# Optimization experiments

Measured on AMD Instinct MI355X. Metric: run time of the kernel, lower is better.

Reference implementation:

```python
import jax, jax.numpy as jnp
import numpy as np

N_NODES = 100000
N_EDGES = 1600000
IN_DIM = 128
HID = 128
OUT_DIM = 64
EPS = 1e-8


def setup_inputs() -> dict:
    key = jax.random.key(0)
    ks = jax.random.split(key, 10)
    x = jax.random.normal(ks[0], (N_NODES, IN_DIM), dtype=jnp.float32)
    edge_index = jax.random.randint(ks[1], (2, N_EDGES), 0, N_NODES, dtype=jnp.int64)
    edge_attr = jax.random.uniform(ks[2], (N_EDGES, 4), dtype=jnp.float32)
    s1 = 1.0 / np.sqrt(IN_DIM)
    s2 = 1.0 / np.sqrt(HID)
    sr = 1.0 / np.sqrt(2 * HID)
    W1 = jax.random.normal(ks[3], (HID, IN_DIM), dtype=jnp.float32) * s1
    b1 = jnp.zeros((HID,), dtype=jnp.float32)
    W2 = jax.random.normal(ks[4], (HID, HID), dtype=jnp.float32) * s2
    b2 = jnp.zeros((HID,), dtype=jnp.float32)
    Wr = jax.random.normal(ks[5], (OUT_DIM, 2 * HID), dtype=jnp.float32) * sr
    br = jnp.zeros((OUT_DIM,), dtype=jnp.float32)
    return {"x": x, "edge_index": edge_index, "edge_attr": edge_attr,
            "W1": W1, "b1": b1, "W2": W2, "b2": b2, "Wr": Wr, "br": br}


def _edge_weight_from_attr_auto(edge_attr):
    # mean over features, min-max normalize, invert, clamp >= 0
    m = edge_attr.mean(axis=-1)                      # [E]
    m_min, m_max = m.min(), m.max()
    m_norm = (m - m_min) / (m_max - m_min + EPS)
    w = jnp.where(m_max - m_min > EPS, 1.0 - m_norm, jnp.ones_like(m))
    return jnp.clip(w, 0.0)


def reference(x, edge_index, edge_attr, W1, b1, W2, b2, Wr, br):
    N = x.shape[0]
    row, col = edge_index[0], edge_index[1]          # source -> target
    ew = _edge_weight_from_attr_auto(edge_attr)      # [E]
    # GCN normalization with self-loops (self-loop weight = 1.0)
    deg = jax.ops.segment_sum(ew, col, num_segments=N) + 1.0   # [N]
    dis = jax.lax.rsqrt(deg)                         # deg >= 1
    norm = dis[row] * ew * dis[col]                  # [E]

    def gcn(h, W, b):
        hW = h @ W.T                                 # [N, d_out]
        agg = jax.ops.segment_sum(norm[:, None] * hW[row], col, num_segments=N)
        # self-loop contribution: dis[i] * 1.0 * dis[i] * hW[i]
        return agg + (dis * dis)[:, None] * hW + b

    # dropout in eval mode -> identity
    h1 = jax.nn.relu(gcn(x, W1, b1))                 # [N, HID]
    h2 = jax.nn.relu(gcn(h1, W2, b2))                # [N, HID]
    hcat = jnp.concatenate([h1, h2], axis=-1)        # [N, 2*HID] (JK concat)
    return hcat @ Wr.T + br                          # residue-level [N, OUT_DIM]
```

## Files before the change

### kernel.cpp

```cpp
#include <hip/hip_runtime.h>

#define NN 100000
#define NE 1600000
#define HID 128
#define ODIM 64
#define NBK 196
#define BSHIFT 9
#define BGRID 512
#define CVTB 48
#define CHUNK 3125
#define BITER 13
#define BINCAP 12288
#define SMAX 4504
#define LMAX 568

typedef unsigned int u32;
typedef unsigned short u16;
typedef __bf16 bf16x8 __attribute__((ext_vector_type(8)));
typedef float f32x4 __attribute__((ext_vector_type(4)));
typedef float f32x2 __attribute__((ext_vector_type(2)));

__device__ __forceinline__ float bf_lo(u32 p){ return __uint_as_float(p << 16); }
__device__ __forceinline__ float bf_hi(u32 p){ return __uint_as_float(p & 0xffff0000u); }
__device__ __forceinline__ u16 f2bf(float f){
  u32 u = __float_as_uint(f);
  u += 0x7fffu + ((u >> 16) & 1u);
  return (u16)(u >> 16);
}
__device__ __forceinline__ bf16x8 ld8bf(const u16* p){ return *(const bf16x8*)p; }
__device__ __forceinline__ bf16x8 cvt8(const float* p){
  union { bf16x8 v; u16 s[8]; } r;
#pragma unroll
  for (int i = 0; i < 8; i++) r.s[i] = f2bf(p[i]);
  return r.v;
}

__global__ __launch_bounds__(256) void k_bin(
    const float* __restrict__ eattr, const int* __restrict__ erow,
    const int* __restrict__ ecol, u32* __restrict__ bcur,
    uint2* __restrict__ bin, u32* __restrict__ minmax,
    const float* __restrict__ W1, const float* __restrict__ W2,
    const float* __restrict__ Wr, u16* __restrict__ W1b,
    u16* __restrict__ W2b, u16* __restrict__ Wrb){
  int tid = threadIdx.x;
  if (blockIdx.x >= BGRID){
    int i = (blockIdx.x - BGRID) * 256 + tid;
    const float* src; u16* dst; int off;
    if (i < 4096){ src = W1; dst = W1b; off = i; }
    else if (i < 8192){ src = W2; dst = W2b; off = i - 4096; }
    else { src = Wr; dst = Wrb; off = i - 8192; }
    float4 v = ((const float4*)src)[off];
    uint2 o;
    o.x = (u32)f2bf(v.x) | ((u32)f2bf(v.y) << 16);
    o.y = (u32)f2bf(v.z) | ((u32)f2bf(v.w) << 16);
    ((uint2*)dst)[off] = o;
    return;
  }
  __shared__ u32 lcnt[NBK], lofs[NBK], gb[NBK];
  __shared__ u32 scn[256];
  __shared__ u16 lmap[LMAX];
  __shared__ uint2 stage[SMAX];
  __shared__ u32 Tt;
  __shared__ float smin[4], smax[4];
  for (int t = tid; t < NBK; t += 256) lcnt[t] = 0;
  __syncthreads();
  int base = blockIdx.x * CHUNK;
  float lmin = __uint_as_float(0x7f800000u), lmax = 0.f;
  u32 pk[BITER]; float mv[BITER]; u32 sv[BITER];
#pragma unroll
  for (int it = 0; it < BITER; it++){
    int idx = it * 256 + tid;
    u32 p = 0xFFFFFFFFu; float m = 0.f; u32 s = 0;
    if (idx < CHUNK){
      int e = base + idx;
      float4 a = ((const float4*)eattr)[e];
      m = 0.25f * (a.x + a.y + a.z + a.w);
      lmin = fminf(lmin, m); lmax = fmaxf(lmax, m);
      int c = ecol[e];
      s = (u32)erow[e]; if (s >= NN) s = 0;
      if ((u32)c < NN){
        u32 b = (u32)c >> BSHIFT;
        u32 r = atomicAdd(&lcnt[b], 1u);
        p = (b << 21) | (((u32)c & 511u) << 12) | r;
      }
    }
    pk[it] = p; mv[it] = m; sv[it] = s;
  }
  __syncthreads();
  u32 na = 0, n = 0;
  if (tid < NBK){ n = lcnt[tid]; na = (n + 7u) & ~7u; }
  scn[tid] = na; __syncthreads();
  for (int s = 1; s < 256; s <<= 1){
    u32 t = (tid >= s) ? scn[tid - s] : 0;
    __syncthreads();
    scn[tid] += t;
    __syncthreads();
  }
  u32 ex = scn[tid] - na;
  if (tid < NBK){
    lofs[tid] = ex;
    u32 g = 0x80000000u;
    if (na){
      u32 gl = atomicAdd(&bcur[tid], na);
      if (gl + na <= BINCAP) g = (u32)tid * BINCAP + gl;
    }
    gb[tid] = g;
    for (u32 l = ex >> 3; l < (ex + na) >> 3; l++) lmap[l] = (u16)tid;
    uint2 sent; sent.x = 0xFFFFFFFFu; sent.y = 0u;
    for (u32 k = n; k < na; k++) stage[ex + k] = sent;
  }
  if (tid == 255) Tt = scn[255];
  __syncthreads();
#pragma unroll
  for (int it = 0; it < BITER; it++){
    u32 p = pk[it];
    if (p == 0xFFFFFFFFu) continue;
    uint2 rec; rec.x = sv[it] | (((p >> 12) & 511u) << 17); rec.y = __float_as_uint(mv[it]);
    stage[lofs[p >> 21] + (p & 4095u)] = rec;
  }
  __syncthreads();
  u32 T = Tt;
  for (u32 i = tid; i < T; i += 256){
    u32 b = lmap[i >> 3];
    u32 g = gb[b];
    if (g != 0x80000000u) bin[g + (i - lofs[b])] = stage[i];
  }
  for (int off = 32; off; off >>= 1){
    lmin = fminf(lmin, __shfl_xor(lmin, off));
    lmax = fmaxf(lmax, __shfl_xor(lmax, off));
  }
  int wid = tid >> 6, lane = tid & 63;
  if (lane == 0){ smin[wid] = lmin; smax[wid] = lmax; }
  __syncthreads();
  if (tid == 0){
    float mn = fminf(fminf(smin[0], smin[1]), fminf(smin[2], smin[3]));
    float mx = fmaxf(fmaxf(smax[0], smax[1]), fmaxf(smax[2], smax[3]));
    atomicMax(&minmax[0], ~__float_as_uint(mn));
    atomicMax(&minmax[1], __float_as_uint(mx));
  }
}

__global__ __launch_bounds__(1024) void k_sort(
    const u32* __restrict__ bcur, const uint2* __restrict__ bin,
    const u32* __restrict__ minmax, u32* __restrict__ csr,
    int* __restrict__ row_start, int* __restrict__ counts, float* __restrict__ dis){
  int b = blockIdx.x;
  int bb = b * BINCAP, be = bb + (int)bcur[b];
  float mn  = __uint_as_float(~minmax[0]);
  float mx  = __uint_as_float(minmax[1]);
  float rng = mx - mn;
  bool flat = !(rng > 1e-8f);
  float inv = 1.f / (rng + 1e-8f);
  __shared__ u32 cnt[512], off[512], cur[512], degfx[512];
  int tid = threadIdx.x;
  if (tid < 512){ cnt[tid] = 0; degfx[tid] = 0; }
  __syncthreads();
  for (int i = bb + tid; i < be; i += 1024){
    uint2 r = bin[i];
    if (r.x == 0xFFFFFFFFu) continue;
    u32 d = (r.x >> 17) & 511u;
    float w = flat ? 1.f : fmaxf(1.f - (__uint_as_float(r.y) - mn) * inv, 0.f);
    atomicAdd(&cnt[d], 1u);
    atomicAdd(&degfx[d], (u32)(w * 1048576.f + 0.5f));
  }
  __syncthreads();
  u32 v = 0;
  if (tid < 512){ v = cnt[tid]; off[tid] = v; }
  __syncthreads();
  for (int s = 1; s < 512; s <<= 1){
    u32 t = 0;
    if (tid < 512 && tid >= s) t = off[tid - s];
    __syncthreads();
    if (tid < 512) off[tid] += t;
    __syncthreads();
  }
  if (tid < 512){
    u32 ex = off[tid] - v;
    cur[tid] = ex;
    int node = (b << BSHIFT) + tid;
    if (node < NN){
      row_start[node] = bb + (int)ex;
      counts[node] = (int)v;
      dis[node] = rsqrtf(1.f + (float)degfx[tid] * (1.f / 1048576.f));
    }
  }
  __syncthreads();
  for (int i = bb + tid; i < be; i += 1024){
    uint2 r = bin[i];
    if (r.x == 0xFFFFFFFFu) continue;
    u32 d = (r.x >> 17) & 511u;
    float w = flat ? 1.f : fmaxf(1.f - (__uint_as_float(r.y) - mn) * inv, 0.f);
    u32 wq = (u32)(w * 32767.f + 0.5f);
    u32 pos = (u32)bb + atomicAdd(&cur[d], 1u);
    csr[pos] = (r.x & 0x1FFFFu) | (wq << 17);
  }
}

template <bool A_F32>
__global__ __launch_bounds__(256) void k_gemm128(
    const void* __restrict__ Av, const u16* __restrict__ Bt,
    const float* __restrict__ dis, u16* __restrict__ G){
  int wave = threadIdx.x >> 6, lane = threadIdx.x & 63;
  int m0 = blockIdx.x * 32;
  int m = lane & 15, q = lane >> 4;
  const float* a0f = (const float*)Av + (size_t)(m0 + m) * HID;
  const float* a1f = a0f + (size_t)16 * HID;
  const u16*   a0b = (const u16*)Av   + (size_t)(m0 + m) * HID;
  const u16*   a1b = a0b + (size_t)16 * HID;
  const u16* brow0 = Bt + (size_t)(wave * 16 + m) * HID;
  const u16* brow1 = brow0 + (size_t)64 * HID;
  f32x4 acc00 = {0.f,0.f,0.f,0.f}, acc01 = {0.f,0.f,0.f,0.f};
  f32x4 acc10 = {0.f,0.f,0.f,0.f}, acc11 = {0.f,0.f,0.f,0.f};
#pragma unroll
  for (int kb = 0; kb < HID; kb += 32){
    bf16x8 af0 = A_F32 ? cvt8(a0f + kb + q * 8) : ld8bf(a0b + kb + q * 8);
    bf16x8 af1 = A_F32 ? cvt8(a1f + kb + q * 8) : ld8bf(a1b + kb + q * 8);
    bf16x8 bf0 = ld8bf(brow0 + kb + q * 8);
    bf16x8 bf1 = ld8bf(brow1 + kb + q * 8);
    acc00 = __builtin_amdgcn_mfma_f32_16x16x32_bf16(af0, bf0, acc00, 0, 0, 0);
    acc01 = __builtin_amdgcn_mfma_f32_16x16x32_bf16(af0, bf1, acc01, 0, 0, 0);
    acc10 = __builtin_amdgcn_mfma_f32_16x16x32_bf16(af1, bf0, acc10, 0, 0, 0);
    acc11 = __builtin_amdgcn_mfma_f32_16x16x32_bf16(af1, bf1, acc11, 0, 0, 0);
  }
  u16* crow0 = G + (size_t)(m0 + q * 4) * HID + wave * 16 + m;
  u16* crow1 = crow0 + (size_t)16 * HID;
#pragma unroll
  for (int r = 0; r < 4; r++){
    float d0 = dis[m0 + q * 4 + r];
    float d1 = dis[m0 + 16 + q * 4 + r];
    crow0[(size_t)r * HID]      = f2bf(acc00[r] * d0);
    crow0[(size_t)r * HID + 64] = f2bf(acc01[r] * d0);
    crow1[(size_t)r * HID]      = f2bf(acc10[r] * d1);
    crow1[(size_t)r * HID + 64] = f2bf(acc11[r] * d1);
  }
}

__global__ __launch_bounds__(256) void k_aggregate(
    const int* __restrict__ row_start, const int* __restrict__ counts,
    const u32* __restrict__ csr, const float* __restrict__ dis,
    const u16* __restrict__ g, const float* __restrict__ bias,
    u16* __restrict__ hout){
  int node = blockIdx.x * 4 + (threadIdx.x >> 6);
  int lane = threadIdx.x & 63;
  int s = row_start[node], c = counts[node];
  const u32* gp = (const u32*)g;
  u32 sv = gp[((size_t)node << 6) + lane];
  f32x2 acc = {bf_lo(sv), bf_hi(sv)};
  for (int base = 0; base < c; base += 64){
    int nch = min(64, c - base);
    u32 sidx = 0; float ws = 0.f;
    if (lane < nch){
      u32 pw = csr[s + base + lane];
      sidx = pw & 0x1FFFFu;
      ws = (float)(pw >> 17) * (1.f / 32767.f);
    }
    u32 wsb = __float_as_uint(ws);
    int j = 0;
#define GATH(T) \
    for (; j + T <= nch; j += T){ \
      u32 pv[T]; float wv[T]; \
      _Pragma("unroll") \
      for (int t = 0; t < T; t++){ \
        u32 st = (u32)__builtin_amdgcn_readlane(sidx, j + t); \
        wv[t] = __uint_as_float(__builtin_amdgcn_readlane(wsb, j + t)); \
        const u32* rowp = gp + st * 64u;          \
        pv[t] = rowp[lane]; \
      } \
      _Pragma("unroll") \
      for (int t = 0; t < T; t++){ \
        f32x2 val = {bf_lo(pv[t]), bf_hi(pv[t])}; \
        acc += wv[t] * val; \
      } \
    }
    GATH(16)
    GATH(8)
    GATH(4)
#undef GATH
    for (; j < nch; ++j){
      u32 st = (u32)__builtin_amdgcn_readlane(sidx, j);
      float wt = __uint_as_float(__builtin_amdgcn_readlane(wsb, j));
      const u32* rowp = gp + st * 64u;
      u32 pv = rowp[lane];
      f32x2 val = {bf_lo(pv), bf_hi(pv)};
      acc += wt * val;
    }
  }
  float di = dis[node];
  float2 bv = ((const float2*)bias)[lane];
  float o0 = fmaxf(acc.x * di + bv.x, 0.f);
  float o1 = fmaxf(acc.y * di + bv.y, 0.f);
  ((u32*)hout)[((size_t)node << 6) + lane] = (u32)f2bf(o0) | ((u32)f2bf(o1) << 16);
}

__global__ __launch_bounds__(256) void k_readout(
    const u16* __restrict__ h1, const u16* __restrict__ h2,
    const u16* __restrict__ Wrb, const float* __restrict__ br, float* __restrict__ out){
  int wave = threadIdx.x >> 6, lane = threadIdx.x & 63;
  int m0 = blockIdx.x * 32;
  int n0 = wave * 16;
  int m = lane & 15, q = lane >> 4;
  const u16* a10 = h1 + (size_t)(m0 + m) * HID;
  const u16* a11 = a10 + (size_t)16 * HID;
  const u16* a20 = h2 + (size_t)(m0 + m) * HID;
  const u16* a21 = a20 + (size_t)16 * HID;
  const u16* b  = Wrb + (size_t)(n0 + m) * (2 * HID);
  f32x4 acc0 = {0.f,0.f,0.f,0.f}, acc1 = {0.f,0.f,0.f,0.f};
#pragma unroll
  for (int kb = 0; kb < HID; kb += 32){
    bf16x8 bf = ld8bf(b + kb + q * 8);
    acc0 = __builtin_amdgcn_mfma_f32_16x16x32_bf16(ld8bf(a10 + kb + q * 8), bf, acc0, 0, 0, 0);
    acc1 = __builtin_amdgcn_mfma_f32_16x16x32_bf16(ld8bf(a11 + kb + q * 8), bf, acc1, 0, 0, 0);
  }
#pragma unroll
  for (int kb = 0; kb < HID; kb += 32){
    bf16x8 bf = ld8bf(b + HID + kb + q * 8);
    acc0 = __builtin_amdgcn_mfma_f32_16x16x32_bf16(ld8bf(a20 + kb + q * 8), bf, acc0, 0, 0, 0);
    acc1 = __builtin_amdgcn_mfma_f32_16x16x32_bf16(ld8bf(a21 + kb + q * 8), bf, acc1, 0, 0, 0);
  }
  float bias = br[n0 + m];
  float* crow0 = out + (size_t)(m0 + q * 4) * ODIM + n0 + m;
  float* crow1 = crow0 + (size_t)16 * ODIM;
#pragma unroll
  for (int r = 0; r < 4; r++){
    crow0[(size_t)r * ODIM] = acc0[r] + bias;
    crow1[(size_t)r * ODIM] = acc1[r] + bias;
  }
}

extern "C" void kernel_launch(void* const* d_in, const int* in_sizes, int n_in,
                              void* d_out, int out_size, void* d_ws, size_t ws_size,
                              hipStream_t stream){
  const float* x     = (const float*)d_in[0];
  const int*   eidx  = (const int*)d_in[1];
  const float* eattr = (const float*)d_in[2];
  const float* W1    = (const float*)d_in[3];
  const float* b1    = (const float*)d_in[4];
  const float* W2    = (const float*)d_in[5];
  const float* b2    = (const float*)d_in[6];
  const float* Wr    = (const float*)d_in[7];
  const float* br    = (const float*)d_in[8];
  const int* erow  = eidx;
  const int* ecol  = eidx + NE;

  char* w = (char*)d_ws;
  auto carve = [&](size_t bytes) -> void* {
    void* p = (void*)w;
    w += (bytes + 255) & ~(size_t)255;
    return p;
  };
  u32* csr       = (u32*)carve((size_t)NBK * BINCAP * 4);
  u32* bcur      = (u32*)carve(256 * 4);
  u32* minmax    = (u32*)carve(256);
  int* row_start = (int*)carve((size_t)NN * 4);
  int* counts    = (int*)carve((size_t)NN * 4);
  float* dis     = (float*)carve((size_t)NN * 4);
  u16* W1b       = (u16*)carve((size_t)HID * HID * 2);
  u16* W2b       = (u16*)carve((size_t)HID * HID * 2);
  u16* Wrb       = (u16*)carve((size_t)ODIM * 2 * HID * 2);
  u16* g         = (u16*)carve((size_t)NN * HID * 2);
  u16* h1        = (u16*)carve((size_t)NN * HID * 2);
  u16* h2        = (u16*)carve((size_t)NN * HID * 2);
  uint2* bin     = (uint2*)h2;

  hipMemsetAsync(bcur, 0, 1024 + 256, stream);
  k_bin<<<BGRID + CVTB, 256, 0, stream>>>(eattr, erow, ecol, bcur, bin, minmax,
                                          W1, W2, Wr, W1b, W2b, Wrb);
  k_sort<<<NBK, 1024, 0, stream>>>(bcur, bin, minmax, csr, row_start, counts, dis);

  k_gemm128<true><<<NN / 32, 256, 0, stream>>>(x, W1b, dis, g);
  k_aggregate<<<NN / 4, 256, 0, stream>>>(row_start, counts, csr, dis, g, b1, h1);
  k_gemm128<false><<<NN / 32, 256, 0, stream>>>(h1, W2b, dis, g);
  k_aggregate<<<NN / 4, 256, 0, stream>>>(row_start, counts, csr, dis, g, b2, h2);
  k_readout<<<NN / 32, 256, 0, stream>>>(h1, h2, Wrb, br, (float*)d_out);
}
```

Measured before the change: 386.3 us.

## Slice feature matrices into 16-column planes for cache-local gathers in aggregation

The intermediate g, h1 and h2 buffers are stored as 8 column slices of 16 bf16 values each ([8][N][16]), and the GEMM and readout kernels read and write this sliced layout. Each aggregation block handles one slice for 16 nodes, and each wave splits 8 edges across lane groups of 8 lanes before combining partial sums with cross-lane shuffles. The aim is to shrink the working set of each gather pass so the randomly gathered rows stay in L2/MALL. In exchange, the CSR list is read 8 times and extra shuffle reductions are added.

```diff
diff --git a/kernel.cpp b/kernel.cpp
--- a/kernel.cpp
+++ b/kernel.cpp
@@ -18,7 +18,6 @@
 typedef unsigned short u16;
 typedef __bf16 bf16x8 __attribute__((ext_vector_type(8)));
 typedef float f32x4 __attribute__((ext_vector_type(4)));
-typedef float f32x2 __attribute__((ext_vector_type(2)));
 
 __device__ __forceinline__ float bf_lo(u32 p){ return __uint_as_float(p << 16); }
 __device__ __forceinline__ float bf_hi(u32 p){ return __uint_as_float(p & 0xffff0000u); }
@@ -34,6 +33,7 @@
   for (int i = 0; i < 8; i++) r.s[i] = f2bf(p[i]);
   return r.v;
 }
+
 
 __global__ __launch_bounds__(256) void k_bin(
     const float* __restrict__ eattr, const int* __restrict__ erow,
@@ -205,33 +205,38 @@
   int m = lane & 15, q = lane >> 4;
   const float* a0f = (const float*)Av + (size_t)(m0 + m) * HID;
   const float* a1f = a0f + (size_t)16 * HID;
-  const u16*   a0b = (const u16*)Av   + (size_t)(m0 + m) * HID;
-  const u16*   a1b = a0b + (size_t)16 * HID;
+  const u16* Ab = (const u16*)Av;
   const u16* brow0 = Bt + (size_t)(wave * 16 + m) * HID;
   const u16* brow1 = brow0 + (size_t)64 * HID;
   f32x4 acc00 = {0.f,0.f,0.f,0.f}, acc01 = {0.f,0.f,0.f,0.f};
   f32x4 acc10 = {0.f,0.f,0.f,0.f}, acc11 = {0.f,0.f,0.f,0.f};
 #pragma unroll
   for (int kb = 0; kb < HID; kb += 32){
-    bf16x8 af0 = A_F32 ? cvt8(a0f + kb + q * 8) : ld8bf(a0b + kb + q * 8);
-    bf16x8 af1 = A_F32 ? cvt8(a1f + kb + q * 8) : ld8bf(a1b + kb + q * 8);
-    bf16x8 bf0 = ld8bf(brow0 + kb + q * 8);
-    bf16x8 bf1 = ld8bf(brow1 + kb + q * 8);
+    int k = kb + q * 8;
+    bf16x8 af0, af1;
+    if (A_F32){
+      af0 = cvt8(a0f + k); af1 = cvt8(a1f + k);
+    } else {
+      const u16* p = Ab + (size_t)(k >> 4) * (NN * 16) + (size_t)(m0 + m) * 16 + (k & 15);
+      af0 = ld8bf(p); af1 = ld8bf(p + 256);
+    }
+    bf16x8 bf0 = ld8bf(brow0 + k);
+    bf16x8 bf1 = ld8bf(brow1 + k);
     acc00 = __builtin_amdgcn_mfma_f32_16x16x32_bf16(af0, bf0, acc00, 0, 0, 0);
     acc01 = __builtin_amdgcn_mfma_f32_16x16x32_bf16(af0, bf1, acc01, 0, 0, 0);
     acc10 = __builtin_amdgcn_mfma_f32_16x16x32_bf16(af1, bf0, acc10, 0, 0, 0);
     acc11 = __builtin_amdgcn_mfma_f32_16x16x32_bf16(af1, bf1, acc11, 0, 0, 0);
   }
-  u16* crow0 = G + (size_t)(m0 + q * 4) * HID + wave * 16 + m;
-  u16* crow1 = crow0 + (size_t)16 * HID;
+  u16* b0 = G + (size_t)wave * (NN * 16) + (size_t)(m0 + q * 4) * 16 + m;
+  u16* b1 = G + (size_t)(wave + 4) * (NN * 16) + (size_t)(m0 + q * 4) * 16 + m;
 #pragma unroll
   for (int r = 0; r < 4; r++){
     float d0 = dis[m0 + q * 4 + r];
     float d1 = dis[m0 + 16 + q * 4 + r];
-    crow0[(size_t)r * HID]      = f2bf(acc00[r] * d0);
-    crow0[(size_t)r * HID + 64] = f2bf(acc01[r] * d0);
-    crow1[(size_t)r * HID]      = f2bf(acc10[r] * d1);
-    crow1[(size_t)r * HID + 64] = f2bf(acc11[r] * d1);
+    b0[r * 16]       = f2bf(acc00[r] * d0);
+    b1[r * 16]       = f2bf(acc01[r] * d0);
+    b0[256 + r * 16] = f2bf(acc10[r] * d1);
+    b1[256 + r * 16] = f2bf(acc11[r] * d1);
   }
 }
 
@@ -240,56 +245,50 @@
     const u32* __restrict__ csr, const float* __restrict__ dis,
     const u16* __restrict__ g, const float* __restrict__ bias,
     u16* __restrict__ hout){
-  int node = blockIdx.x * 4 + (threadIdx.x >> 6);
+  int s = blockIdx.x & 7;
+  int node0 = (blockIdx.x >> 3) * 16 + (threadIdx.x >> 6) * 4;
   int lane = threadIdx.x & 63;
-  int s = row_start[node], c = counts[node];
-  const u32* gp = (const u32*)g;
-  u32 sv = gp[((size_t)node << 6) + lane];
-  f32x2 acc = {bf_lo(sv), bf_hi(sv)};
-  for (int base = 0; base < c; base += 64){
-    int nch = min(64, c - base);
-    u32 sidx = 0; float ws = 0.f;
-    if (lane < nch){
-      u32 pw = csr[s + base + lane];
-      sidx = pw & 0x1FFFFu;
-      ws = (float)(pw >> 17) * (1.f / 32767.f);
-    }
-    u32 wsb = __float_as_uint(ws);
-    int j = 0;
-#define GATH(T) \
-    for (; j + T <= nch; j += T){ \
-      u32 pv[T]; float wv[T]; \
-      _Pragma("unroll") \
-      for (int t = 0; t < T; t++){ \
-        u32 st = (u32)__builtin_amdgcn_readlane(sidx, j + t); \
-        wv[t] = __uint_as_float(__builtin_amdgcn_readlane(wsb, j + t)); \
-        const u32* rowp = gp + st * 64u;          \
-        pv[t] = rowp[lane]; \
-      } \
-      _Pragma("unroll") \
-      for (int t = 0; t < T; t++){ \
-        f32x2 val = {bf_lo(pv[t]), bf_hi(pv[t])}; \
-        acc += wv[t] * val; \
-      } \
-    }
-    GATH(16)
-    GATH(8)
-    GATH(4)
-#undef GATH
-    for (; j < nch; ++j){
-      u32 st = (u32)__builtin_amdgcn_readlane(sidx, j);
-      float wt = __uint_as_float(__builtin_amdgcn_readlane(wsb, j));
-      const u32* rowp = gp + st * 64u;
-      u32 pv = rowp[lane];
-      f32x2 val = {bf_lo(pv), bf_hi(pv)};
-      acc += wt * val;
-    }
-  }
-  float di = dis[node];
-  float2 bv = ((const float2*)bias)[lane];
-  float o0 = fmaxf(acc.x * di + bv.x, 0.f);
-  float o1 = fmaxf(acc.y * di + bv.y, 0.f);
-  ((u32*)hout)[((size_t)node << 6) + lane] = (u32)f2bf(o0) | ((u32)f2bf(o1) << 16);
+  int sub = lane & 7, egrp = lane >> 3;
+  const u32* gs = (const u32*)g + (size_t)s * (NN * 8);
+  u32* hs = (u32*)hout + (size_t)s * (NN * 8);
+  float2 bv = ((const float2*)bias)[s * 8 + sub];
+#pragma unroll
+  for (int nn = 0; nn < 4; nn++){
+    int node = node0 + nn;
+    int srow = row_start[node], c = counts[node];
+    float a0 = 0.f, a1 = 0.f;
+    for (int base = 0; base < c; base += 64){
+      int nch = min(64, c - base);
+      int pwAll = 0;
+      if (lane < nch) pwAll = (int)__builtin_nontemporal_load(&csr[srow + base + lane]);
+      int j = 0;
+      for (; j + 16 <= nch; j += 16){
+        u32 pw0 = (u32)__shfl(pwAll, j + egrp);
+        u32 pw1 = (u32)__shfl(pwAll, j + 8 + egrp);
+        u32 pv0 = gs[(pw0 & 0x1FFFFu) * 8u + sub];
+        u32 pv1 = gs[(pw1 & 0x1FFFFu) * 8u + sub];
+        float w0 = (float)(pw0 >> 17) * (1.f / 32767.f);
+        float w1 = (float)(pw1 >> 17) * (1.f / 32767.f);
+        a0 += w0 * bf_lo(pv0); a1 += w0 * bf_hi(pv0);
+        a0 += w1 * bf_lo(pv1); a1 += w1 * bf_hi(pv1);
+      }
+      for (; j < nch; j += 8){
+        u32 pw = (u32)__shfl(pwAll, j + egrp);
+        u32 pv = gs[(pw & 0x1FFFFu) * 8u + sub];
+        float w = (float)(pw >> 17) * (1.f / 32767.f);
+        a0 += w * bf_lo(pv); a1 += w * bf_hi(pv);
+      }
+    }
+    a0 += __shfl_xor(a0, 8);  a1 += __shfl_xor(a1, 8);
+    a0 += __shfl_xor(a0, 16); a1 += __shfl_xor(a1, 16);
+    a0 += __shfl_xor(a0, 32); a1 += __shfl_xor(a1, 32);
+    u32 sv = gs[(u32)node * 8u + sub];
+    float di = dis[node];
+    float o0 = fmaxf((a0 + bf_lo(sv)) * di + bv.x, 0.f);
+    float o1 = fmaxf((a1 + bf_hi(sv)) * di + bv.y, 0.f);
+    if (egrp == 0)
+      hs[(u32)node * 8u + sub] = (u32)f2bf(o0) | ((u32)f2bf(o1) << 16);
+  }
 }
 
 __global__ __launch_bounds__(256) void k_readout(
@@ -299,23 +298,23 @@
   int m0 = blockIdx.x * 32;
   int n0 = wave * 16;
   int m = lane & 15, q = lane >> 4;
-  const u16* a10 = h1 + (size_t)(m0 + m) * HID;
-  const u16* a11 = a10 + (size_t)16 * HID;
-  const u16* a20 = h2 + (size_t)(m0 + m) * HID;
-  const u16* a21 = a20 + (size_t)16 * HID;
-  const u16* b  = Wrb + (size_t)(n0 + m) * (2 * HID);
+  const u16* b = Wrb + (size_t)(n0 + m) * (2 * HID);
   f32x4 acc0 = {0.f,0.f,0.f,0.f}, acc1 = {0.f,0.f,0.f,0.f};
 #pragma unroll
   for (int kb = 0; kb < HID; kb += 32){
-    bf16x8 bf = ld8bf(b + kb + q * 8);
-    acc0 = __builtin_amdgcn_mfma_f32_16x16x32_bf16(ld8bf(a10 + kb + q * 8), bf, acc0, 0, 0, 0);
-    acc1 = __builtin_amdgcn_mfma_f32_16x16x32_bf16(ld8bf(a11 + kb + q * 8), bf, acc1, 0, 0, 0);
+    int k = kb + q * 8;
+    const u16* p = h1 + (size_t)(k >> 4) * (NN * 16) + (size_t)(m0 + m) * 16 + (k & 15);
+    bf16x8 bf = ld8bf(b + k);
+    acc0 = __builtin_amdgcn_mfma_f32_16x16x32_bf16(ld8bf(p), bf, acc0, 0, 0, 0);
+    acc1 = __builtin_amdgcn_mfma_f32_16x16x32_bf16(ld8bf(p + 256), bf, acc1, 0, 0, 0);
   }
 #pragma unroll
   for (int kb = 0; kb < HID; kb += 32){
-    bf16x8 bf = ld8bf(b + HID + kb + q * 8);
-    acc0 = __builtin_amdgcn_mfma_f32_16x16x32_bf16(ld8bf(a20 + kb + q * 8), bf, acc0, 0, 0, 0);
-    acc1 = __builtin_amdgcn_mfma_f32_16x16x32_bf16(ld8bf(a21 + kb + q * 8), bf, acc1, 0, 0, 0);
+    int k = kb + q * 8;
+    const u16* p = h2 + (size_t)(k >> 4) * (NN * 16) + (size_t)(m0 + m) * 16 + (k & 15);
+    bf16x8 bf = ld8bf(b + HID + k);
+    acc0 = __builtin_amdgcn_mfma_f32_16x16x32_bf16(ld8bf(p), bf, acc0, 0, 0, 0);
+    acc1 = __builtin_amdgcn_mfma_f32_16x16x32_bf16(ld8bf(p + 256), bf, acc1, 0, 0, 0);
   }
   float bias = br[n0 + m];
   float* crow0 = out + (size_t)(m0 + q * 4) * ODIM + n0 + m;
@@ -368,8 +367,8 @@
   k_sort<<<NBK, 1024, 0, stream>>>(bcur, bin, minmax, csr, row_start, counts, dis);
 
   k_gemm128<true><<<NN / 32, 256, 0, stream>>>(x, W1b, dis, g);
-  k_aggregate<<<NN / 4, 256, 0, stream>>>(row_start, counts, csr, dis, g, b1, h1);
+  k_aggregate<<<(NN / 16) * 8, 256, 0, stream>>>(row_start, counts, csr, dis, g, b1, h1);
   k_gemm128<false><<<NN / 32, 256, 0, stream>>>(h1, W2b, dis, g);
-  k_aggregate<<<NN / 4, 256, 0, stream>>>(row_start, counts, csr, dis, g, b2, h2);
+  k_aggregate<<<(NN / 16) * 8, 256, 0, stream>>>(row_start, counts, csr, dis, g, b2, h2);
   k_readout<<<NN / 32, 256, 0, stream>>>(h1, h2, Wrb, br, (float*)d_out);
 }
```

Measured after the change: 744.3 us. 1.93x slower.
